# Kernel tuning notes

Hardware: AMD Instinct MI355X
Metric: run time of the kernel (lower is better)

Reference implementation:

```python
import jax, jax.numpy as jnp
import numpy as np

K = 5          # kernel_size
PAD = (K - 1) // 2  # fixed_padding with dilation=1, stride=1 -> 'same'


def setup_inputs() -> dict:
    key = jax.random.key(0)
    kx, kw = jax.random.split(key)
    x = jax.random.normal(kx, (4, 8, 512, 512), dtype=jnp.float32)
    # nn.Parameter initialized to zeros in the original; use small random values
    # so the op is non-trivial (math is identical for any weight values).
    weight = jax.random.normal(kw, (8, 8, K, K), dtype=jnp.float32) * 0.05
    return {"x": x, "weight": weight}


def reference(x, weight):
    """Morphological dilation2d with hard max (soft_max=False).

    out[n,o,h,w] = max_{c,dy,dx} ( x_pad[n,c,h+dy,w+dx] + weight[o,c,dy,dx] )
    Faithful to: pad zeros -> unfold -> weight + x -> max over dim C*k*k.
    Computed as a fused sliding-window max-plus reduction (no (N,C,k,k,H,W)
    unfold tensor is materialized; loop is over the fixed k*k kernel taps).
    """
    N, C, H, W = x.shape
    O = weight.shape[0]
    xp = jnp.pad(x, ((0, 0), (0, 0), (PAD, PAD), (PAD, PAD)))  # zero pad, as in F.pad
    out = jnp.full((N, O, H, W), -jnp.inf, dtype=x.dtype)
    for dy in range(K):
        for dx in range(K):
            patch = xp[:, :, dy:dy + H, dx:dx + W]           # (N,C,H,W)
            w_tap = weight[:, :, dy, dx]                      # (O,C)
            # (N,1,C,H,W) + (1,O,C,1,1) -> max over C -> (N,O,H,W)
            term = patch[:, None] + w_tap[None, :, :, None, None]
            out = jnp.maximum(out, jnp.max(term, axis=2))
    return out
```

## Files before the change

### kernel.cpp

```cpp
#include <hip/hip_runtime.h>
#include <math.h>
#include <stdint.h>

typedef _Float16 half2v __attribute__((ext_vector_type(2)));

#define KK 5
#define PADK 2
#define C_IN 8
#define O_OUT 8
#define HH 512
#define WW 512
#define TH 8
#define TW 128
#define LROWS (TH + 2 * PADK)
#define LPAIRS 68
#define NW (O_OUT * C_IN * KK * KK)
#define WROW (O_OUT * KK)

static __device__ __forceinline__ half2v bc_h2(uint32_t u) {
    return __builtin_bit_cast(half2v, u);
}
static __device__ __forceinline__ half2v emax(half2v a, half2v b) {
    return __builtin_elementwise_max(a, b);
}

__global__ void prep_weights_kernel(const float* __restrict__ w,
                                    uint32_t* __restrict__ wp) {
    int i = blockIdx.x * 256 + threadIdx.x;
    if (i < NW) {
        int dx = i % KK;
        int t  = i / KK;
        int dy = t % KK;  t /= KK;
        int c  = t % C_IN;
        int o  = t / C_IN;
        _Float16 h = (_Float16)w[i];
        uint16_t hb = __builtin_bit_cast(uint16_t, h);
        int j = ((c * KK + dy) * O_OUT + o) * KK + dx;
        wp[j] = ((uint32_t)hb << 16) | (uint32_t)hb;
    }
}

template <bool USE_WS>
__global__ __launch_bounds__(512, 8)
void dil_kernel(const float* __restrict__ x,
                const float* __restrict__ wf,
                const uint32_t* __restrict__ wp,
                float* __restrict__ out) {
    __shared__ uint32_t lds[C_IN][LROWS][LPAIRS];

    const int tid = threadIdx.x;
    const int w0 = blockIdx.x * TW;
    const int h0 = blockIdx.y * TH;
    const int n  = blockIdx.z;

    const float* xn = x + (size_t)n * (C_IN * HH * WW);
    for (int idx = tid; idx < C_IN * LROWS * LPAIRS; idx += 512) {
        int c   = idx / (LROWS * LPAIRS);
        int rem = idx - c * (LROWS * LPAIRS);
        int r   = rem / LPAIRS;
        int jp  = rem - r * LPAIRS;
        int gh = h0 - PADK + r;
        int gw = w0 - PADK + 2 * jp;
        float v0 = 0.f, v1 = 0.f;
        if ((unsigned)gh < (unsigned)HH) {
            const float* row = xn + ((size_t)c * HH + gh) * WW;
            if ((unsigned)gw < (unsigned)WW) v0 = row[gw];
            if ((unsigned)(gw + 1) < (unsigned)WW) v1 = row[gw + 1];
        }
        _Float16 a = (_Float16)v0, b = (_Float16)v1;
        uint32_t u = ((uint32_t)__builtin_bit_cast(uint16_t, b) << 16) |
                     (uint32_t)__builtin_bit_cast(uint16_t, a);
        (&lds[0][0][0])[idx] = u;
    }
    __syncthreads();

    const int tx  = tid & 63;
    const int wid = __builtin_amdgcn_readfirstlane(tid >> 6);

    const uint32_t NINF = 0xFC00FC00u;
    half2v acc[O_OUT];
    #pragma unroll
    for (int o = 0; o < O_OUT; ++o) acc[o] = bc_h2(NINF);

    for (int ci = 0; ci < C_IN; ++ci) {
        const int c = (ci + wid) & 7;

        uint32_t u[KK][3];
        #pragma unroll
        for (int dy = 0; dy < KK; ++dy) {
            const uint32_t* lrow = &lds[c][wid + dy][tx];
            u[dy][0] = lrow[0];
            u[dy][1] = lrow[1];
            u[dy][2] = lrow[2];
        }

        const uint32_t* wc = wp + c * (KK * WROW);
        #pragma unroll
        for (int dy = 0; dy < KK; ++dy) {
            uint32_t wrow[WROW];
            const uint32_t* wd = wc + dy * WROW;
            #pragma unroll
            for (int k = 0; k < WROW; ++k) {
                if (USE_WS) {
                    wrow[k] = wd[k];
                } else {
                    int o  = k / KK;
                    int dx = k - o * KK;
                    const int off = ((o * C_IN + c) * KK + dy) * KK + dx;
                    _Float16 h = (_Float16)wf[off];
                    uint16_t hb = __builtin_bit_cast(uint16_t, h);
                    wrow[k] = ((uint32_t)hb << 16) | (uint32_t)hb;
                }
            }

            uint32_t u0 = u[dy][0], u1 = u[dy][1], u2 = u[dy][2];
            uint32_t s0 = (u0 >> 16) | (u1 << 16);
            uint32_t s1 = (u1 >> 16) | (u2 << 16);
            half2v H0 = bc_h2(u0), H1 = bc_h2(u1), H2 = bc_h2(u2);
            half2v S0 = bc_h2(s0), S1 = bc_h2(s1);

            #pragma unroll
            for (int o = 0; o < O_OUT; ++o) {
                half2v W0 = bc_h2(wrow[o * KK + 0]);
                half2v W1 = bc_h2(wrow[o * KK + 1]);
                half2v W2 = bc_h2(wrow[o * KK + 2]);
                half2v W3 = bc_h2(wrow[o * KK + 3]);
                half2v W4 = bc_h2(wrow[o * KK + 4]);
                half2v t0 = H0 + W0, t1 = S0 + W1, t2 = H1 + W2,
                       t3 = S1 + W3, t4 = H2 + W4;
                half2v m01 = emax(t0, t1), m23 = emax(t2, t3);
                acc[o] = emax(acc[o], emax(emax(m01, m23), t4));
            }
        }
    }

    float* onp = out + (size_t)n * (O_OUT * HH * WW);
    const int h = h0 + wid;
    const int wcol = w0 + 2 * tx;
    #pragma unroll
    for (int o = 0; o < O_OUT; ++o) {
        float2 r;
        r.x = (float)acc[o].x;
        r.y = (float)acc[o].y;
        *(float2*)(&onp[((size_t)o * HH + h) * WW + wcol]) = r;
    }
}

extern "C" void kernel_launch(void* const* d_in, const int* in_sizes, int n_in,
                              void* d_out, int out_size, void* d_ws, size_t ws_size,
                              hipStream_t stream) {
    const float* x   = (const float*)d_in[0];
    const float* wgt = (const float*)d_in[1];
    float* out = (float*)d_out;

    dim3 grid(WW / TW, HH / TH, 4);
    dim3 block(512);

    if (ws_size >= (size_t)NW * 4) {
        uint32_t* wp = (uint32_t*)d_ws;
        prep_weights_kernel<<<(NW + 255) / 256, 256, 0, stream>>>(wgt, wp);
        dil_kernel<true><<<grid, block, 0, stream>>>(x, wgt, wp, out);
    } else {
        dil_kernel<false><<<grid, block, 0, stream>>>(x, wgt, nullptr, out);
    }
}
```

Baseline: 74.46 us.

## Double-buffer per-row weights in VGPRs and use inline packed fp16 asm

Weights are now loaded as 16-byte vectors into VGPRs through a forced-VGPR pointer, so the loads become vector rather than scalar. They are double-buffered so the next row's weights are prefetched while the current row computes. The add and max steps are written as inline v_pk_add_f16/v_pk_max_f16 asm, and the channel loop is unrolled by two. Launch bounds drop to 4 blocks per SM to make room for the 80 extra weight registers per thread, which may lower occupancy and raise per-lane vector load traffic.

Measured after the change: 118.1 us. 58.6% more time.

```diff
diff --git a/kernel.cpp b/kernel.cpp
--- a/kernel.cpp
+++ b/kernel.cpp
@@ -2,7 +2,9 @@
 #include <math.h>
 #include <stdint.h>
 
+typedef uint32_t u32;
 typedef _Float16 half2v __attribute__((ext_vector_type(2)));
+typedef uint32_t u32x4 __attribute__((ext_vector_type(4)));
 
 #define KK 5
 #define PADK 2
@@ -17,15 +19,18 @@
 #define NW (O_OUT * C_IN * KK * KK)
 #define WROW (O_OUT * KK)
 
-static __device__ __forceinline__ half2v bc_h2(uint32_t u) {
+static __device__ __forceinline__ half2v bc_h2(u32 u) {
     return __builtin_bit_cast(half2v, u);
 }
-static __device__ __forceinline__ half2v emax(half2v a, half2v b) {
-    return __builtin_elementwise_max(a, b);
+static __device__ __forceinline__ u32 pk_add(u32 a, u32 b) {
+    u32 d; asm("v_pk_add_f16 %0, %1, %2" : "=v"(d) : "v"(a), "v"(b)); return d;
+}
+static __device__ __forceinline__ u32 pk_max(u32 a, u32 b) {
+    u32 d; asm("v_pk_max_f16 %0, %1, %2" : "=v"(d) : "v"(a), "v"(b)); return d;
 }
 
 __global__ void prep_weights_kernel(const float* __restrict__ w,
-                                    uint32_t* __restrict__ wp) {
+                                    u32* __restrict__ wp) {
     int i = blockIdx.x * 256 + threadIdx.x;
     if (i < NW) {
         int dx = i % KK;
@@ -36,17 +41,42 @@
         _Float16 h = (_Float16)w[i];
         uint16_t hb = __builtin_bit_cast(uint16_t, h);
         int j = ((c * KK + dy) * O_OUT + o) * KK + dx;
-        wp[j] = ((uint32_t)hb << 16) | (uint32_t)hb;
+        wp[j] = ((u32)hb << 16) | (u32)hb;
     }
 }
 
 template <bool USE_WS>
-__global__ __launch_bounds__(512, 8)
+static __device__ __forceinline__ void loadw(u32x4 (&dst)[10], const u32* wq,
+                                             int c, int dy,
+                                             const float* wf) {
+    if constexpr (USE_WS) {
+        uintptr_t q = (uintptr_t)(wq + (c * KK + dy) * WROW);
+        asm("" : "+v"(q));
+        const u32x4* p = (const u32x4*)q;
+        #pragma unroll
+        for (int k = 0; k < 10; ++k) dst[k] = p[k];
+    } else {
+        #pragma unroll
+        for (int o = 0; o < O_OUT; ++o) {
+            #pragma unroll
+            for (int dx = 0; dx < KK; ++dx) {
+                float f = wf[((o * C_IN + c) * KK + dy) * KK + dx];
+                _Float16 h = (_Float16)f;
+                uint16_t hb = __builtin_bit_cast(uint16_t, h);
+                int k = o * KK + dx;
+                dst[k >> 2][k & 3] = ((u32)hb << 16) | (u32)hb;
+            }
+        }
+    }
+}
+
+template <bool USE_WS>
+__global__ __launch_bounds__(512, 4)
 void dil_kernel(const float* __restrict__ x,
                 const float* __restrict__ wf,
-                const uint32_t* __restrict__ wp,
+                const u32* __restrict__ wq,
                 float* __restrict__ out) {
-    __shared__ uint32_t lds[C_IN][LROWS][LPAIRS];
+    __shared__ u32 lds[C_IN][LROWS][LPAIRS];
 
     const int tid = threadIdx.x;
     const int w0 = blockIdx.x * TW;
@@ -68,80 +98,72 @@
             if ((unsigned)(gw + 1) < (unsigned)WW) v1 = row[gw + 1];
         }
         _Float16 a = (_Float16)v0, b = (_Float16)v1;
-        uint32_t u = ((uint32_t)__builtin_bit_cast(uint16_t, b) << 16) |
-                     (uint32_t)__builtin_bit_cast(uint16_t, a);
+        u32 u = ((u32)__builtin_bit_cast(uint16_t, b) << 16) |
+                (u32)__builtin_bit_cast(uint16_t, a);
         (&lds[0][0][0])[idx] = u;
     }
     __syncthreads();
 
     const int tx  = tid & 63;
-    const int wid = __builtin_amdgcn_readfirstlane(tid >> 6);
+    const int wid = tid >> 6;
 
-    const uint32_t NINF = 0xFC00FC00u;
-    half2v acc[O_OUT];
+    u32 acc[O_OUT];
     #pragma unroll
-    for (int o = 0; o < O_OUT; ++o) acc[o] = bc_h2(NINF);
+    for (int o = 0; o < O_OUT; ++o) acc[o] = 0xFC00FC00u;
 
-    for (int ci = 0; ci < C_IN; ++ci) {
-        const int c = (ci + wid) & 7;
+#define DYB(dy_, B) { \
+    u32 u0 = u_[dy_][0], u1 = u_[dy_][1], u2 = u_[dy_][2]; \
+    u32 s0 = (u0 >> 16) | (u1 << 16); \
+    u32 s1 = (u1 >> 16) | (u2 << 16); \
+    _Pragma("unroll") \
+    for (int o = 0; o < O_OUT; ++o) { \
+        u32 t0 = pk_add(B[(o*5+0)>>2][(o*5+0)&3], u0); \
+        u32 t1 = pk_add(B[(o*5+1)>>2][(o*5+1)&3], s0); \
+        u32 t2 = pk_add(B[(o*5+2)>>2][(o*5+2)&3], u1); \
+        u32 t3 = pk_add(B[(o*5+3)>>2][(o*5+3)&3], s1); \
+        u32 t4 = pk_add(B[(o*5+4)>>2][(o*5+4)&3], u2); \
+        acc[o] = pk_max(acc[o], \
+                 pk_max(pk_max(pk_max(t0, t1), pk_max(t2, t3)), t4)); \
+    } \
+}
 
-        uint32_t u[KK][3];
-        #pragma unroll
-        for (int dy = 0; dy < KK; ++dy) {
-            const uint32_t* lrow = &lds[c][wid + dy][tx];
-            u[dy][0] = lrow[0];
-            u[dy][1] = lrow[1];
-            u[dy][2] = lrow[2];
-        }
+#define CSTEP(c_, cn_, B0, B1) { \
+    u32 u_[KK][3]; \
+    _Pragma("unroll") \
+    for (int dy = 0; dy < KK; ++dy) { \
+        const u32* lrow = &lds[c_][wid + dy][tx]; \
+        u_[dy][0] = lrow[0]; u_[dy][1] = lrow[1]; u_[dy][2] = lrow[2]; \
+    } \
+    loadw<USE_WS>(B1, wq, c_, 1, wf);  DYB(0, B0) \
+    loadw<USE_WS>(B0, wq, c_, 2, wf);  DYB(1, B1) \
+    loadw<USE_WS>(B1, wq, c_, 3, wf);  DYB(2, B0) \
+    loadw<USE_WS>(B0, wq, c_, 4, wf);  DYB(3, B1) \
+    loadw<USE_WS>(B1, wq, cn_, 0, wf); DYB(4, B0) \
+}
 
-        const uint32_t* wc = wp + c * (KK * WROW);
-        #pragma unroll
-        for (int dy = 0; dy < KK; ++dy) {
-            uint32_t wrow[WROW];
-            const uint32_t* wd = wc + dy * WROW;
-            #pragma unroll
-            for (int k = 0; k < WROW; ++k) {
-                if (USE_WS) {
-                    wrow[k] = wd[k];
-                } else {
-                    int o  = k / KK;
-                    int dx = k - o * KK;
-                    const int off = ((o * C_IN + c) * KK + dy) * KK + dx;
-                    _Float16 h = (_Float16)wf[off];
-                    uint16_t hb = __builtin_bit_cast(uint16_t, h);
-                    wrow[k] = ((uint32_t)hb << 16) | (uint32_t)hb;
-                }
-            }
+    u32x4 wrA[10], wrB[10];
+    const int c0 = wid & 7;
+    loadw<USE_WS>(wrA, wq, c0, 0, wf);
 
-            uint32_t u0 = u[dy][0], u1 = u[dy][1], u2 = u[dy][2];
-            uint32_t s0 = (u0 >> 16) | (u1 << 16);
-            uint32_t s1 = (u1 >> 16) | (u2 << 16);
-            half2v H0 = bc_h2(u0), H1 = bc_h2(u1), H2 = bc_h2(u2);
-            half2v S0 = bc_h2(s0), S1 = bc_h2(s1);
-
-            #pragma unroll
-            for (int o = 0; o < O_OUT; ++o) {
-                half2v W0 = bc_h2(wrow[o * KK + 0]);
-                half2v W1 = bc_h2(wrow[o * KK + 1]);
-                half2v W2 = bc_h2(wrow[o * KK + 2]);
-                half2v W3 = bc_h2(wrow[o * KK + 3]);
-                half2v W4 = bc_h2(wrow[o * KK + 4]);
-                half2v t0 = H0 + W0, t1 = S0 + W1, t2 = H1 + W2,
-                       t3 = S1 + W3, t4 = H2 + W4;
-                half2v m01 = emax(t0, t1), m23 = emax(t2, t3);
-                acc[o] = emax(acc[o], emax(emax(m01, m23), t4));
-            }
-        }
+    for (int cb = 0; cb < C_IN; cb += 2) {
+        const int cA = (cb + 0 + wid) & 7;
+        const int cB = (cb + 1 + wid) & 7;
+        const int cC = (cb + 2 + wid) & 7;
+        CSTEP(cA, cB, wrA, wrB)
+        CSTEP(cB, cC, wrB, wrA)
     }
+#undef CSTEP
+#undef DYB
 
     float* onp = out + (size_t)n * (O_OUT * HH * WW);
     const int h = h0 + wid;
     const int wcol = w0 + 2 * tx;
     #pragma unroll
     for (int o = 0; o < O_OUT; ++o) {
+        half2v a = bc_h2(acc[o]);
         float2 r;
-        r.x = (float)acc[o].x;
-        r.y = (float)acc[o].y;
+        r.x = (float)a.x;
+        r.y = (float)a.y;
         *(float2*)(&onp[((size_t)o * HH + h) * WW + wcol]) = r;
     }
 }
@@ -157,7 +179,7 @@
     dim3 block(512);
 
     if (ws_size >= (size_t)NW * 4) {
-        uint32_t* wp = (uint32_t*)d_ws;
+        u32* wp = (u32*)d_ws;
         prep_weights_kernel<<<(NW + 255) / 256, 256, 0, stream>>>(wgt, wp);
         dil_kernel<true><<<grid, block, 0, stream>>>(x, wgt, wp, out);
     } else {
```
